# Optimization experiments

Hardware: AMD Instinct MI355X
Metric: run time of the kernel (lower is better)

Reference implementation:

```python
import jax, jax.numpy as jnp
import numpy as np

EPS = 1e-08

def setup_inputs() -> dict:
    key = jax.random.key(0)
    kq, kk, kv = jax.random.split(key, 3)
    B, H, S, D = 2, 16, 2048, 64
    q = jax.random.normal(kq, (B, H, S, D), dtype=jnp.float32)
    k = jax.random.normal(kk, (B, H, S, D), dtype=jnp.float32)
    v = jax.random.normal(kv, (B, H, S, D), dtype=jnp.float32)
    return {"q": q, "k": k, "v": v}

def reference(q, k, v):
    d_k = q.shape[-1]
    # scores: [B,H,S,S]
    scores = jnp.einsum('bhqd,bhkd->bhqk', q, k) / jnp.sqrt(jnp.asarray(d_k, q.dtype))
    attn_weights = jax.nn.softmax(scores, axis=-1)
    # output: [B,H,S,D]
    output = jnp.einsum('bhqk,bhkd->bhqd', attn_weights, v)
    # non-differentiable row-norm preconditioner C_ii = 1/||A[i]||_2
    row_norms = jnp.linalg.norm(jax.lax.stop_gradient(output), axis=-1, keepdims=True)
    preconditioned_output = output / (row_norms + EPS)
    return (preconditioned_output, attn_weights)
```

## Files before the change

kernel.cpp:

```cpp
#include <hip/hip_runtime.h>

#define SS 2048
#define DD 64
#define S2 0.18033688011112042f

typedef __attribute__((ext_vector_type(4))) float f32x4;
typedef __attribute__((ext_vector_type(8))) short bfx8;
typedef __attribute__((ext_vector_type(4))) short bfx4;

__device__ __forceinline__ short f2bf(float f) {
    unsigned u = __builtin_bit_cast(unsigned, f);
    u += 0x7fffu + ((u >> 16) & 1u);
    return (short)(u >> 16);
}
__device__ __forceinline__ bfx8 pack8(f32x4 a, f32x4 b) {
    bfx8 r;
    r[0] = f2bf(a[0]); r[1] = f2bf(a[1]); r[2] = f2bf(a[2]); r[3] = f2bf(a[3]);
    r[4] = f2bf(b[0]); r[5] = f2bf(b[1]); r[6] = f2bf(b[2]); r[7] = f2bf(b[3]);
    return r;
}
__device__ __forceinline__ float bf2f(short s) {
    unsigned u = ((unsigned)(unsigned short)s) << 16;
    return __builtin_bit_cast(float, u);
}
__device__ __forceinline__ void bar_raw() {
    asm volatile("s_barrier" ::: "memory");
    __builtin_amdgcn_sched_barrier(0);
}
__device__ __forceinline__ void wait_vm0() {
    asm volatile("s_waitcnt vmcnt(0)" ::: "memory");
    __builtin_amdgcn_sched_barrier(0);
}
__device__ __forceinline__ void wait_vm2() {
    asm volatile("s_waitcnt vmcnt(2)" ::: "memory");
    __builtin_amdgcn_sched_barrier(0);
}
__device__ __forceinline__ void wait_vm8() {
    asm volatile("s_waitcnt vmcnt(8)" ::: "memory");
    __builtin_amdgcn_sched_barrier(0);
}
__device__ __forceinline__ void gload16(const void* g, void* l) {
    __builtin_amdgcn_global_load_lds(
        (const __attribute__((address_space(1))) unsigned*)g,
        (__attribute__((address_space(3))) unsigned*)l, 16, 0, 0);
}

__global__ __launch_bounds__(256) void prep_kernel(
    const float* __restrict__ k, const float* __restrict__ v,
    short* __restrict__ kbf, short* __restrict__ vtbf)
{
    const int blk = blockIdx.x;
    const int bh = blk >> 4, kc = blk & 15;
    const int tid = threadIdx.x;
    const long hoff = (long)bh * SS * DD;

    {
        const int key = tid >> 1, h = tid & 1;
        const float* kp = k + hoff + (long)(kc * 128 + key) * DD + h * 32;
        char* krow = (char*)kbf + ((long)bh * SS + kc * 128 + key) * 128;
        const int x = (key & 3) << 5;
        #pragma unroll
        for (int i = 0; i < 4; ++i) {
            f32x4 a = *(const f32x4*)(kp + i * 8);
            f32x4 b = *(const f32x4*)(kp + i * 8 + 4);
            *(bfx8*)(krow + ((h * 64 + i * 16) ^ x)) = pack8(a, b);
        }
    }

    __shared__ __align__(16) short Vl[64][136];
    {
        const int kq = (tid & 31) * 4, dg = (tid >> 5) * 8;
        const float* vp = v + hoff + (long)(kc * 128 + kq) * DD + dg;
        f32x4 r0a = *(const f32x4*)(vp),        r0b = *(const f32x4*)(vp + 4);
        f32x4 r1a = *(const f32x4*)(vp + DD),   r1b = *(const f32x4*)(vp + DD + 4);
        f32x4 r2a = *(const f32x4*)(vp + 2*DD), r2b = *(const f32x4*)(vp + 2*DD + 4);
        f32x4 r3a = *(const f32x4*)(vp + 3*DD), r3b = *(const f32x4*)(vp + 3*DD + 4);
        #pragma unroll
        for (int d = 0; d < 4; ++d) {
            bfx4 w;
            w[0] = f2bf(r0a[d]); w[1] = f2bf(r1a[d]);
            w[2] = f2bf(r2a[d]); w[3] = f2bf(r3a[d]);
            *(bfx4*)&Vl[dg + d][kq] = w;
        }
        #pragma unroll
        for (int d = 0; d < 4; ++d) {
            bfx4 w;
            w[0] = f2bf(r0b[d]); w[1] = f2bf(r1b[d]);
            w[2] = f2bf(r2b[d]); w[3] = f2bf(r3b[d]);
            *(bfx4*)&Vl[dg + 4 + d][kq] = w;
        }
    }
    __syncthreads();
    {
        const int d = tid >> 2, quar = tid & 3;
        char* vrow = (char*)vtbf + ((long)bh * 64 + d) * 4096 + kc * 256;
        const int x = (d & 3) << 5;
        #pragma unroll
        for (int i = 0; i < 4; ++i) {
            bfx8 w = *(const bfx8*)((const char*)&Vl[d][0] + quar * 64 + i * 16);
            *(bfx8*)(vrow + ((quar * 64 + i * 16) ^ x)) = w;
        }
    }
}

__global__ __launch_bounds__(256, 3) void pattn_main(
    const float* __restrict__ q, const short* __restrict__ kbf,
    const short* __restrict__ vtbf, float* __restrict__ out,
    float* __restrict__ attn)
{
    const int blk = blockIdx.x;
    const int bh  = (blk & 7) * 4 + ((blk >> 3) & 3);
    const int qt  = blk >> 5;
    const int tid = threadIdx.x;
    const int wid = tid >> 6, lane = tid & 63;
    const int c = lane & 15, g = lane >> 4;

    __shared__ __align__(16) short Kl[2][64][64];
    __shared__ __align__(16) short Vt[2][64][64];
    __shared__ __align__(16) short Wc[4][16][80];

    const long hoff = (long)bh * SS * DD;
    const int  qrow = qt * 64 + wid * 16 + c;

    bfx8 bq0, bq1;
    {
        const float* qp = q + hoff + (long)qrow * DD + 8 * g;
        f32x4 x0 = *(const f32x4*)(qp)      * S2;
        f32x4 x1 = *(const f32x4*)(qp + 4)  * S2;
        f32x4 x2 = *(const f32x4*)(qp + 32) * S2;
        f32x4 x3 = *(const f32x4*)(qp + 36) * S2;
        bq0 = pack8(x0, x1);
        bq1 = pack8(x2, x3);
    }

    const char* kb_base = (const char*)kbf + (long)bh * SS * 128;
    const char* vt_base = (const char*)vtbf + (long)bh * 64 * 4096;
    const int soff = wid * 2048 + lane * 16;

    auto issueK = [&](int kt, int b) {
        const char* gsrc = kb_base + (long)kt * 128 + soff;
        char* ldst = (char*)&Kl[b][0][0] + wid * 2048;
        gload16(gsrc, ldst);
        gload16(gsrc + 1024, ldst + 1024);
    };
    auto issueV = [&](int kt, int b) {
        #pragma unroll
        for (int j = 0; j < 2; ++j) {
            const int off = soff + j * 1024;
            const char* gsrc = vt_base + (long)(off >> 7) * 4096 + (long)kt * 2 + (off & 127);
            gload16(gsrc, (char*)&Vt[b][0][0] + wid * 2048 + j * 1024);
        }
    };

    float lsum = 0.f;
    issueK(0, 0);
    wait_vm0(); bar_raw();
    for (int it = 0; it < 32; ++it) {
        const int p = it & 1;
        issueK(((it + 1) & 31) * 64, p ^ 1);
        wait_vm2(); bar_raw();
        #pragma unroll
        for (int t = 0; t < 4; ++t) {
            const int row = t * 16 + c;
            const char* kr = (const char*)&Kl[p][row][0];
            const int x = (row & 3) << 5;
            bfx8 ka = *(const bfx8*)(kr + ((16 * g) ^ x));
            bfx8 kb = *(const bfx8*)(kr + ((64 + 16 * g) ^ x));
            f32x4 s = {0.f, 0.f, 0.f, 0.f};
            s = __builtin_amdgcn_mfma_f32_16x16x32_bf16(ka, bq0, s, 0, 0, 0);
            s = __builtin_amdgcn_mfma_f32_16x16x32_bf16(kb, bq1, s, 0, 0, 0);
            lsum += __builtin_amdgcn_exp2f(s[0]);
            lsum += __builtin_amdgcn_exp2f(s[1]);
            lsum += __builtin_amdgcn_exp2f(s[2]);
            lsum += __builtin_amdgcn_exp2f(s[3]);
        }
        bar_raw();
    }
    lsum += __shfl_xor(lsum, 16, 64);
    lsum += __shfl_xor(lsum, 32, 64);
    const float invl = 1.0f / lsum;

    f32x4 acc[4];
    #pragma unroll
    for (int i = 0; i < 4; ++i) acc[i] = (f32x4){0.f, 0.f, 0.f, 0.f};

    float* attnw = attn + (long)bh * SS * SS + (long)(qt * 64 + wid * 16) * SS;

    issueV(0, 0);
    wait_vm0(); bar_raw();
    for (int it = 0; it < 32; ++it) {
        const int p  = it & 1;
        const int k0 = it * 64;
        const int nk = ((it + 1) & 31) * 64;
        issueK(nk, p ^ 1);
        issueV(nk, p ^ 1);
        wait_vm8();
        bar_raw();

        #pragma unroll
        for (int half = 0; half < 2; ++half) {
            #pragma unroll
            for (int tt = 0; tt < 2; ++tt) {
                const int t = half * 2 + tt;
                const int row = t * 16 + c;
                const char* kr = (const char*)&Kl[p][row][0];
                const int x = (row & 3) << 5;
                bfx8 ka = *(const bfx8*)(kr + ((16 * g) ^ x));
                bfx8 kb = *(const bfx8*)(kr + ((64 + 16 * g) ^ x));
                f32x4 s = {0.f, 0.f, 0.f, 0.f};
                s = __builtin_amdgcn_mfma_f32_16x16x32_bf16(ka, bq0, s, 0, 0, 0);
                s = __builtin_amdgcn_mfma_f32_16x16x32_bf16(kb, bq1, s, 0, 0, 0);
                bfx4 wp;
                wp[0] = f2bf(__builtin_amdgcn_exp2f(s[0]) * invl);
                wp[1] = f2bf(__builtin_amdgcn_exp2f(s[1]) * invl);
                wp[2] = f2bf(__builtin_amdgcn_exp2f(s[2]) * invl);
                wp[3] = f2bf(__builtin_amdgcn_exp2f(s[3]) * invl);
                *(bfx4*)&Wc[wid][c][t * 16 + 4 * g] = wp;
            }
            bfx8 wb = *(const bfx8*)((const char*)&Wc[wid][c][0] + half * 64 + 16 * g);
            #pragma unroll
            for (int ds = 0; ds < 4; ++ds) {
                const int vrow = ds * 16 + c;
                bfx8 va = *(const bfx8*)((const char*)&Vt[p][vrow][0] +
                                         ((half * 64 + 16 * g) ^ ((vrow & 3) << 5)));
                acc[ds] = __builtin_amdgcn_mfma_f32_16x16x32_bf16(va, wb, acc[ds], 0, 0, 0);
            }
        }

        {
            const int col4 = c * 4;
            #pragma unroll
            for (int rg = 0; rg < 4; ++rg) {
                const int r = rg * 4 + g;
                bfx4 w4 = *(const bfx4*)&Wc[wid][r][col4];
                f32x4 o;
                o[0] = bf2f(w4[0]); o[1] = bf2f(w4[1]);
                o[2] = bf2f(w4[2]); o[3] = bf2f(w4[3]);
                __builtin_nontemporal_store(o, (f32x4*)(attnw + (long)r * SS + k0 + col4));
            }
        }
        bar_raw();
    }

    float ssq = 0.f;
    #pragma unroll
    for (int ds = 0; ds < 4; ++ds)
        #pragma unroll
        for (int r = 0; r < 4; ++r)
            ssq += acc[ds][r] * acc[ds][r];
    ssq += __shfl_xor(ssq, 16, 64);
    ssq += __shfl_xor(ssq, 32, 64);
    const float inv = 1.0f / (sqrtf(ssq) + 1e-8f);

    float* op = out + hoff + (long)qrow * DD;
    #pragma unroll
    for (int ds = 0; ds < 4; ++ds) {
        f32x4 o;
        o[0] = acc[ds][0] * inv; o[1] = acc[ds][1] * inv;
        o[2] = acc[ds][2] * inv; o[3] = acc[ds][3] * inv;
        *(f32x4*)&op[ds * 16 + 4 * g] = o;
    }
}

__device__ __forceinline__ void fb_bar_lg() {
    asm volatile("s_waitcnt lgkmcnt(0)\n\ts_barrier" ::: "memory");
    __builtin_amdgcn_sched_barrier(0);
}
__global__ __launch_bounds__(256, 3) void pattn_fallback(
    const float* __restrict__ q, const float* __restrict__ k,
    const float* __restrict__ v, float* __restrict__ out,
    float* __restrict__ attn)
{
    const int blk = blockIdx.x;
    const int bh  = (blk & 7) * 4 + ((blk >> 3) & 3);
    const int qt  = blk >> 5;
    const int tid = threadIdx.x;
    const int wid = tid >> 6, lane = tid & 63;
    const int c = lane & 15, g = lane >> 4;

    const long hoff = (long)bh * SS * DD;
    const int  qrow = qt * 64 + wid * 16 + c;

    __shared__ __align__(16) short Kl[128][72];
    __shared__ __align__(16) short Vt[64][136];
    __shared__ __align__(16) short Wc[4][16][136];

    bfx8 bq0, bq1;
    {
        const float* qp = q + hoff + (long)qrow * DD + 8 * g;
        f32x4 x0 = *(const f32x4*)(qp)      * S2;
        f32x4 x1 = *(const f32x4*)(qp + 4)  * S2;
        f32x4 x2 = *(const f32x4*)(qp + 32) * S2;
        f32x4 x3 = *(const f32x4*)(qp + 36) * S2;
        bq0 = pack8(x0, x1);
        bq1 = pack8(x2, x3);
    }

    const int skey = tid >> 1, sdh = (tid & 1) << 5;
    const int vkq  = (tid & 31) * 4, vdg = (tid >> 5) * 8;
    f32x4 kr[8], vr[8];

    auto loadK = [&](int k0) {
        const float* kp = k + hoff + (long)(k0 + skey) * DD + sdh;
        #pragma unroll
        for (int i = 0; i < 8; ++i) kr[i] = *(const f32x4*)(kp + 4 * i);
    };
    auto writeK = [&]() {
        *(bfx8*)&Kl[skey][sdh + 0]  = pack8(kr[0], kr[1]);
        *(bfx8*)&Kl[skey][sdh + 8]  = pack8(kr[2], kr[3]);
        *(bfx8*)&Kl[skey][sdh + 16] = pack8(kr[4], kr[5]);
        *(bfx8*)&Kl[skey][sdh + 24] = pack8(kr[6], kr[7]);
    };
    auto loadV = [&](int k0) {
        const float* vp = v + hoff + (long)(k0 + vkq) * DD + vdg;
        #pragma unroll
        for (int r = 0; r < 4; ++r) {
            vr[2 * r]     = *(const f32x4*)(vp + r * DD);
            vr[2 * r + 1] = *(const f32x4*)(vp + r * DD + 4);
        }
    };
    auto writeV = [&]() {
        #pragma unroll
        for (int d = 0; d < 4; ++d) {
            bfx4 w;
            w[0] = f2bf(vr[0][d]); w[1] = f2bf(vr[2][d]);
            w[2] = f2bf(vr[4][d]); w[3] = f2bf(vr[6][d]);
            *(bfx4*)&Vt[vdg + d][vkq] = w;
        }
        #pragma unroll
        for (int d = 0; d < 4; ++d) {
            bfx4 w;
            w[0] = f2bf(vr[1][d]); w[1] = f2bf(vr[3][d]);
            w[2] = f2bf(vr[5][d]); w[3] = f2bf(vr[7][d]);
            *(bfx4*)&Vt[vdg + 4 + d][vkq] = w;
        }
    };

    float lsum = 0.f;
    loadK(0); wait_vm0(); writeK();
    for (int it = 0; it < 16; ++it) {
        fb_bar_lg();
        if (it < 15) loadK((it + 1) * 128);
        #pragma unroll
        for (int T = 0; T < 8; ++T) {
            bfx8 ka = *(const bfx8*)&Kl[T * 16 + c][8 * g];
            bfx8 kb = *(const bfx8*)&Kl[T * 16 + c][32 + 8 * g];
            f32x4 s = {0.f, 0.f, 0.f, 0.f};
            s = __builtin_amdgcn_mfma_f32_16x16x32_bf16(ka, bq0, s, 0, 0, 0);
            s = __builtin_amdgcn_mfma_f32_16x16x32_bf16(kb, bq1, s, 0, 0, 0);
            lsum += __builtin_amdgcn_exp2f(s[0]);
            lsum += __builtin_amdgcn_exp2f(s[1]);
            lsum += __builtin_amdgcn_exp2f(s[2]);
            lsum += __builtin_amdgcn_exp2f(s[3]);
        }
        if (it < 15) wait_vm0();
        bar_raw();
        if (it < 15) writeK();
    }
    lsum += __shfl_xor(lsum, 16, 64);
    lsum += __shfl_xor(lsum, 32, 64);
    const float invl = 1.0f / lsum;

    f32x4 acc[4];
    #pragma unroll
    for (int i = 0; i < 4; ++i) acc[i] = (f32x4){0.f, 0.f, 0.f, 0.f};

    float* attnw = attn + (long)bh * SS * SS + (long)(qt * 64 + wid * 16) * SS;

    loadK(0); loadV(0);
    wait_vm0();
    bar_raw();
    writeK(); writeV();
    for (int it = 0; it < 16; ++it) {
        const int k0 = it * 128;
        fb_bar_lg();
        if (it < 15) { loadK(k0 + 128); loadV(k0 + 128); }

        #pragma unroll
        for (int G = 0; G < 4; ++G) {
            #pragma unroll
            for (int t = 0; t < 2; ++t) {
                const int kb2 = G * 32 + t * 16;
                bfx8 ka = *(const bfx8*)&Kl[kb2 + c][8 * g];
                bfx8 kb = *(const bfx8*)&Kl[kb2 + c][32 + 8 * g];
                f32x4 s = {0.f, 0.f, 0.f, 0.f};
                s = __builtin_amdgcn_mfma_f32_16x16x32_bf16(ka, bq0, s, 0, 0, 0);
                s = __builtin_amdgcn_mfma_f32_16x16x32_bf16(kb, bq1, s, 0, 0, 0);
                bfx4 wp;
                wp[0] = f2bf(__builtin_amdgcn_exp2f(s[0]) * invl);
                wp[1] = f2bf(__builtin_amdgcn_exp2f(s[1]) * invl);
                wp[2] = f2bf(__builtin_amdgcn_exp2f(s[2]) * invl);
                wp[3] = f2bf(__builtin_amdgcn_exp2f(s[3]) * invl);
                *(bfx4*)&Wc[wid][c][kb2 + 4 * g] = wp;
            }
            bfx8 wb = *(const bfx8*)&Wc[wid][c][G * 32 + 8 * g];
            #pragma unroll
            for (int ds = 0; ds < 4; ++ds) {
                bfx8 va = *(const bfx8*)&Vt[ds * 16 + c][G * 32 + 8 * g];
                acc[ds] = __builtin_amdgcn_mfma_f32_16x16x32_bf16(va, wb, acc[ds], 0, 0, 0);
            }
        }

        {
            const int half = lane >> 5;
            const int col  = (lane & 31) * 4;
            #pragma unroll
            for (int rg = 0; rg < 8; ++rg) {
                const int r = rg * 2 + half;
                bfx4 w4 = *(const bfx4*)&Wc[wid][r][col];
                f32x4 o;
                o[0] = bf2f(w4[0]); o[1] = bf2f(w4[1]);
                o[2] = bf2f(w4[2]); o[3] = bf2f(w4[3]);
                __builtin_nontemporal_store(o, (f32x4*)(attnw + (long)r * SS + k0 + col));
            }
        }

        if (it < 15) {
            wait_vm8();
            bar_raw();
            writeK(); writeV();
        }
    }

    float ssq = 0.f;
    #pragma unroll
    for (int ds = 0; ds < 4; ++ds)
        #pragma unroll
        for (int r = 0; r < 4; ++r)
            ssq += acc[ds][r] * acc[ds][r];
    ssq += __shfl_xor(ssq, 16, 64);
    ssq += __shfl_xor(ssq, 32, 64);
    const float inv = 1.0f / (sqrtf(ssq) + 1e-8f);

    float* op = out + hoff + (long)qrow * DD;
    #pragma unroll
    for (int ds = 0; ds < 4; ++ds) {
        f32x4 o;
        o[0] = acc[ds][0] * inv; o[1] = acc[ds][1] * inv;
        o[2] = acc[ds][2] * inv; o[3] = acc[ds][3] * inv;
        *(f32x4*)&op[ds * 16 + 4 * g] = o;
    }
}

extern "C" void kernel_launch(void* const* d_in, const int* in_sizes, int n_in,
                              void* d_out, int out_size, void* d_ws, size_t ws_size,
                              hipStream_t stream) {
    const float* q = (const float*)d_in[0];
    const float* k = (const float*)d_in[1];
    const float* v = (const float*)d_in[2];
    float* out  = (float*)d_out;
    float* attn = out + (long)2 * 16 * SS * DD;

    const size_t need = 2UL * 32 * SS * DD * sizeof(short);
    if (ws_size >= need) {
        short* kbf  = (short*)d_ws;
        short* vtbf = kbf + (size_t)32 * SS * DD;
        hipLaunchKernelGGL(prep_kernel, dim3(512), dim3(256), 0, stream, k, v, kbf, vtbf);
        hipLaunchKernelGGL(pattn_main, dim3(1024), dim3(256), 0, stream, q, kbf, vtbf, out, attn);
    } else {
        hipLaunchKernelGGL(pattn_fallback, dim3(1024), dim3(256), 0, stream, q, k, v, out, attn);
    }
}
```

Baseline: 192.0 us.

## Process two 16-row query tiles per wave to reuse K/V fragments

Each wave now handles 32 query rows instead of 16, so each block covers 128 rows and the grid is halved. Every K and V fragment loaded from LDS feeds two MFMA chains, which halves the global and LDS traffic for K/V per query row. In exchange, register use per thread roughly doubles (launch bounds drop from 3 to 2 blocks) and the grid shrinks to 512 blocks, which reduces parallelism and latency hiding for the large attention-weight store.

```diff
diff --git a/kernel.cpp b/kernel.cpp
--- a/kernel.cpp
+++ b/kernel.cpp
@@ -103,7 +103,7 @@
     }
 }
 
-__global__ __launch_bounds__(256, 3) void pattn_main(
+__global__ __launch_bounds__(256, 2) void pattn_main2(
     const float* __restrict__ q, const short* __restrict__ kbf,
     const short* __restrict__ vtbf, float* __restrict__ out,
     float* __restrict__ attn)
@@ -117,20 +117,20 @@
 
     __shared__ __align__(16) short Kl[2][64][64];
     __shared__ __align__(16) short Vt[2][64][64];
-    __shared__ __align__(16) short Wc[4][16][80];
+    __shared__ __align__(16) short Wc[4][32][80];
 
     const long hoff = (long)bh * SS * DD;
-    const int  qrow = qt * 64 + wid * 16 + c;
-
-    bfx8 bq0, bq1;
+    const int  qA = qt * 128 + wid * 32 + c;
+    const int  qB = qA + 16;
+
+    bfx8 bqA0, bqA1, bqB0, bqB1;
     {
-        const float* qp = q + hoff + (long)qrow * DD + 8 * g;
-        f32x4 x0 = *(const f32x4*)(qp)      * S2;
-        f32x4 x1 = *(const f32x4*)(qp + 4)  * S2;
-        f32x4 x2 = *(const f32x4*)(qp + 32) * S2;
-        f32x4 x3 = *(const f32x4*)(qp + 36) * S2;
-        bq0 = pack8(x0, x1);
-        bq1 = pack8(x2, x3);
+        const float* qp = q + hoff + (long)qA * DD + 8 * g;
+        bqA0 = pack8(*(const f32x4*)(qp)      * S2, *(const f32x4*)(qp + 4)  * S2);
+        bqA1 = pack8(*(const f32x4*)(qp + 32) * S2, *(const f32x4*)(qp + 36) * S2);
+        const float* qp2 = q + hoff + (long)qB * DD + 8 * g;
+        bqB0 = pack8(*(const f32x4*)(qp2)      * S2, *(const f32x4*)(qp2 + 4)  * S2);
+        bqB1 = pack8(*(const f32x4*)(qp2 + 32) * S2, *(const f32x4*)(qp2 + 36) * S2);
     }
 
     const char* kb_base = (const char*)kbf + (long)bh * SS * 128;
@@ -152,7 +152,7 @@
         }
     };
 
-    float lsum = 0.f;
+    float lsA[4] = {0.f,0.f,0.f,0.f}, lsB[4] = {0.f,0.f,0.f,0.f};
     issueK(0, 0);
     wait_vm0(); bar_raw();
     for (int it = 0; it < 32; ++it) {
@@ -166,25 +166,33 @@
             const int x = (row & 3) << 5;
             bfx8 ka = *(const bfx8*)(kr + ((16 * g) ^ x));
             bfx8 kb = *(const bfx8*)(kr + ((64 + 16 * g) ^ x));
-            f32x4 s = {0.f, 0.f, 0.f, 0.f};
-            s = __builtin_amdgcn_mfma_f32_16x16x32_bf16(ka, bq0, s, 0, 0, 0);
-            s = __builtin_amdgcn_mfma_f32_16x16x32_bf16(kb, bq1, s, 0, 0, 0);
-            lsum += __builtin_amdgcn_exp2f(s[0]);
-            lsum += __builtin_amdgcn_exp2f(s[1]);
-            lsum += __builtin_amdgcn_exp2f(s[2]);
-            lsum += __builtin_amdgcn_exp2f(s[3]);
+            f32x4 sA = {0.f,0.f,0.f,0.f}, sB = {0.f,0.f,0.f,0.f};
+            sA = __builtin_amdgcn_mfma_f32_16x16x32_bf16(ka, bqA0, sA, 0, 0, 0);
+            sA = __builtin_amdgcn_mfma_f32_16x16x32_bf16(kb, bqA1, sA, 0, 0, 0);
+            sB = __builtin_amdgcn_mfma_f32_16x16x32_bf16(ka, bqB0, sB, 0, 0, 0);
+            sB = __builtin_amdgcn_mfma_f32_16x16x32_bf16(kb, bqB1, sB, 0, 0, 0);
+            #pragma unroll
+            for (int r = 0; r < 4; ++r) {
+                lsA[r] += __builtin_amdgcn_exp2f(sA[r]);
+                lsB[r] += __builtin_amdgcn_exp2f(sB[r]);
+            }
         }
         bar_raw();
     }
-    lsum += __shfl_xor(lsum, 16, 64);
-    lsum += __shfl_xor(lsum, 32, 64);
-    const float invl = 1.0f / lsum;
-
-    f32x4 acc[4];
-    #pragma unroll
-    for (int i = 0; i < 4; ++i) acc[i] = (f32x4){0.f, 0.f, 0.f, 0.f};
-
-    float* attnw = attn + (long)bh * SS * SS + (long)(qt * 64 + wid * 16) * SS;
+    float lsumA = (lsA[0] + lsA[1]) + (lsA[2] + lsA[3]);
+    float lsumB = (lsB[0] + lsB[1]) + (lsB[2] + lsB[3]);
+    lsumA += __shfl_xor(lsumA, 16, 64);
+    lsumA += __shfl_xor(lsumA, 32, 64);
+    lsumB += __shfl_xor(lsumB, 16, 64);
+    lsumB += __shfl_xor(lsumB, 32, 64);
+    const float invlA = 1.0f / lsumA;
+    const float invlB = 1.0f / lsumB;
+
+    f32x4 accA[4], accB[4];
+    #pragma unroll
+    for (int i = 0; i < 4; ++i) { accA[i] = (f32x4){0.f,0.f,0.f,0.f}; accB[i] = (f32x4){0.f,0.f,0.f,0.f}; }
+
+    float* attnw = attn + (long)bh * SS * SS + (long)(qt * 128 + wid * 32) * SS;
 
     issueV(0, 0);
     wait_vm0(); bar_raw();
@@ -207,30 +215,36 @@
                 const int x = (row & 3) << 5;
                 bfx8 ka = *(const bfx8*)(kr + ((16 * g) ^ x));
                 bfx8 kb = *(const bfx8*)(kr + ((64 + 16 * g) ^ x));
-                f32x4 s = {0.f, 0.f, 0.f, 0.f};
-                s = __builtin_amdgcn_mfma_f32_16x16x32_bf16(ka, bq0, s, 0, 0, 0);
-                s = __builtin_amdgcn_mfma_f32_16x16x32_bf16(kb, bq1, s, 0, 0, 0);
-                bfx4 wp;
-                wp[0] = f2bf(__builtin_amdgcn_exp2f(s[0]) * invl);
-                wp[1] = f2bf(__builtin_amdgcn_exp2f(s[1]) * invl);
-                wp[2] = f2bf(__builtin_amdgcn_exp2f(s[2]) * invl);
-                wp[3] = f2bf(__builtin_amdgcn_exp2f(s[3]) * invl);
-                *(bfx4*)&Wc[wid][c][t * 16 + 4 * g] = wp;
-            }
-            bfx8 wb = *(const bfx8*)((const char*)&Wc[wid][c][0] + half * 64 + 16 * g);
+                f32x4 sA = {0.f,0.f,0.f,0.f}, sB = {0.f,0.f,0.f,0.f};
+                sA = __builtin_amdgcn_mfma_f32_16x16x32_bf16(ka, bqA0, sA, 0, 0, 0);
+                sA = __builtin_amdgcn_mfma_f32_16x16x32_bf16(kb, bqA1, sA, 0, 0, 0);
+                sB = __builtin_amdgcn_mfma_f32_16x16x32_bf16(ka, bqB0, sB, 0, 0, 0);
+                sB = __builtin_amdgcn_mfma_f32_16x16x32_bf16(kb, bqB1, sB, 0, 0, 0);
+                bfx4 wpA, wpB;
+                #pragma unroll
+                for (int r = 0; r < 4; ++r) {
+                    wpA[r] = f2bf(__builtin_amdgcn_exp2f(sA[r]) * invlA);
+                    wpB[r] = f2bf(__builtin_amdgcn_exp2f(sB[r]) * invlB);
+                }
+                *(bfx4*)&Wc[wid][c][t * 16 + 4 * g]      = wpA;
+                *(bfx4*)&Wc[wid][16 + c][t * 16 + 4 * g] = wpB;
+            }
+            bfx8 wbA = *(const bfx8*)((const char*)&Wc[wid][c][0]      + half * 64 + 16 * g);
+            bfx8 wbB = *(const bfx8*)((const char*)&Wc[wid][16 + c][0] + half * 64 + 16 * g);
             #pragma unroll
             for (int ds = 0; ds < 4; ++ds) {
                 const int vrow = ds * 16 + c;
                 bfx8 va = *(const bfx8*)((const char*)&Vt[p][vrow][0] +
                                          ((half * 64 + 16 * g) ^ ((vrow & 3) << 5)));
-                acc[ds] = __builtin_amdgcn_mfma_f32_16x16x32_bf16(va, wb, acc[ds], 0, 0, 0);
+                accA[ds] = __builtin_amdgcn_mfma_f32_16x16x32_bf16(va, wbA, accA[ds], 0, 0, 0);
+                accB[ds] = __builtin_amdgcn_mfma_f32_16x16x32_bf16(va, wbB, accB[ds], 0, 0, 0);
             }
         }
 
         {
             const int col4 = c * 4;
             #pragma unroll
-            for (int rg = 0; rg < 4; ++rg) {
+            for (int rg = 0; rg < 8; ++rg) {
                 const int r = rg * 4 + g;
                 bfx4 w4 = *(const bfx4*)&Wc[wid][r][col4];
                 f32x4 o;
@@ -242,23 +256,27 @@
         bar_raw();
     }
 
-    float ssq = 0.f;
+    float ssqA = 0.f, ssqB = 0.f;
     #pragma unroll
     for (int ds = 0; ds < 4; ++ds)
         #pragma unroll
-        for (int r = 0; r < 4; ++r)
-            ssq += acc[ds][r] * acc[ds][r];
-    ssq += __shfl_xor(ssq, 16, 64);
-    ssq += __shfl_xor(ssq, 32, 64);
-    const float inv = 1.0f / (sqrtf(ssq) + 1e-8f);
-
-    float* op = out + hoff + (long)qrow * DD;
+        for (int r = 0; r < 4; ++r) { ssqA += accA[ds][r] * accA[ds][r]; ssqB += accB[ds][r] * accB[ds][r]; }
+    ssqA += __shfl_xor(ssqA, 16, 64);
+    ssqA += __shfl_xor(ssqA, 32, 64);
+    ssqB += __shfl_xor(ssqB, 16, 64);
+    ssqB += __shfl_xor(ssqB, 32, 64);
+    const float invA = 1.0f / (sqrtf(ssqA) + 1e-8f);
+    const float invB = 1.0f / (sqrtf(ssqB) + 1e-8f);
+
+    float* opA = out + hoff + (long)qA * DD;
+    float* opB = out + hoff + (long)qB * DD;
     #pragma unroll
     for (int ds = 0; ds < 4; ++ds) {
-        f32x4 o;
-        o[0] = acc[ds][0] * inv; o[1] = acc[ds][1] * inv;
-        o[2] = acc[ds][2] * inv; o[3] = acc[ds][3] * inv;
-        *(f32x4*)&op[ds * 16 + 4 * g] = o;
+        f32x4 oA, oB;
+        #pragma unroll
+        for (int r = 0; r < 4; ++r) { oA[r] = accA[ds][r] * invA; oB[r] = accB[ds][r] * invB; }
+        *(f32x4*)&opA[ds * 16 + 4 * g] = oA;
+        *(f32x4*)&opB[ds * 16 + 4 * g] = oB;
     }
 }
 
@@ -456,7 +474,7 @@
         short* kbf  = (short*)d_ws;
         short* vtbf = kbf + (size_t)32 * SS * DD;
         hipLaunchKernelGGL(prep_kernel, dim3(512), dim3(256), 0, stream, k, v, kbf, vtbf);
-        hipLaunchKernelGGL(pattn_main, dim3(1024), dim3(256), 0, stream, q, kbf, vtbf, out, attn);
+        hipLaunchKernelGGL(pattn_main2, dim3(512), dim3(256), 0, stream, q, kbf, vtbf, out, attn);
     } else {
         hipLaunchKernelGGL(pattn_fallback, dim3(1024), dim3(256), 0, stream, q, k, v, out, attn);
     }
```

New measurement: 173.6 us, median of 2. 9.6% less time.
